# Optimization experiments

Hardware: AMD Instinct MI355X
Metric: run time of the kernel (lower is better)

The kernel has to match this reference:

```python
import jax, jax.numpy as jnp
import numpy as np

N = 100000      # nodes
E = 1600000     # edges (avg degree 16)
IN = 128        # in_channels
H = 128         # hidden_channels
OUT = 64        # out_channels
NHID = 3        # num_layers (hidden->hidden SAGE convs)


def _lin(k, fan_out, fan_in):
    s = 1.0 / np.sqrt(fan_in)
    return jax.random.uniform(k, (fan_out, fan_in), jnp.float32, -s, s)


def setup_inputs() -> dict:
    key = jax.random.key(0)
    ks = jax.random.split(key, 12)
    x = jax.random.normal(ks[0], (N, IN), dtype=jnp.float32)
    edge_index = jax.random.randint(ks[1], (2, E), 0, N, dtype=jnp.int32)
    # inProj Linear(IN -> H)
    Wp = _lin(ks[2], H, IN)
    bp = jnp.zeros((H,), jnp.float32)
    # 3 hidden SAGEConv(H -> H): lin_l (with bias) on aggregated neighbors, lin_r (no bias) on root
    Wl_h = jnp.stack([_lin(jax.random.fold_in(ks[3], i), H, H) for i in range(NHID)])
    bl_h = jnp.zeros((NHID, H), jnp.float32)
    Wr_h = jnp.stack([_lin(jax.random.fold_in(ks[4], i), H, H) for i in range(NHID)])
    # output SAGEConv(H -> OUT)
    Wl_o = _lin(ks[5], OUT, H)
    bl_o = jnp.zeros((OUT,), jnp.float32)
    Wr_o = _lin(ks[6], OUT, H)
    return {"x": x, "edge_index": edge_index, "Wp": Wp, "bp": bp,
            "Wl_h": Wl_h, "bl_h": bl_h, "Wr_h": Wr_h,
            "Wl_o": Wl_o, "bl_o": bl_o, "Wr_o": Wr_o}


def reference(x, edge_index, Wp, bp, Wl_h, bl_h, Wr_h, Wl_o, bl_o, Wr_o):
    src, dst = edge_index[0], edge_index[1]
    ones = jnp.ones((E,), x.dtype)
    deg = jax.ops.segment_sum(ones, dst, num_segments=N)           # [N]
    inv_deg = (1.0 / jnp.maximum(deg, 1.0))[:, None]               # [N,1]

    def sage(h, Wl, bl, Wr):
        # mean aggregation of source features onto destinations (irregular gather+scatter)
        s = jax.ops.segment_sum(h[src], dst, num_segments=N)       # [N,d]
        mean = s * inv_deg
        return mean @ Wl.T + bl + h @ Wr.T

    h = x @ Wp.T + bp
    inp = h
    h = jax.nn.relu(h)
    for i in range(NHID):
        h = sage(h, Wl_h[i], bl_h[i], Wr_h[i])
        h = jax.nn.relu(h)                                          # dropout is identity in eval
        h = h + 0.2 * inp
    h = sage(h, Wl_o, bl_o, Wr_o)
    return jax.nn.log_softmax(h, axis=-1)
```

## Files before the change

kernel.cpp:

```cpp
#include <hip/hip_runtime.h>
#include <math.h>

#define N_NODES 100000
#define N_EDGES 1600000
#define NBUK 391
#define PCHUNK 8192
#define NPBLK 196
#define PBLK16 3128

typedef unsigned short u16;
typedef unsigned char u8;
typedef __bf16 bf16x8 __attribute__((ext_vector_type(8)));
typedef float f32x4 __attribute__((ext_vector_type(4)));
typedef float f32x2 __attribute__((ext_vector_type(2)));

#define OFF_RP      0u
#define OFF_INVDEG  400016u
#define OFF_BHIST   800016u
#define OFF_BBASE   801600u
#define OFF_GCUR    803200u
#define OFF_PCTR    804800u
#define OFF_PAIRS   805056u
#define OFF_COL     13605056u
#define OFF_PACK    20005056u
#define OFF_INP     20267200u
#define OFF_H       45867200u
#define OFF_H8A     71467200u
#define OFF_H8B     84267200u
#define OFF_GL      97067200u
#define OFF_GR      109867200u
#define OFF_MEAN    122667200u
#define WS_NEEDED   148267200u

#define PK_WP   0
#define PK_WL   16384
#define PK_WR   65536
#define PK_WLO  114688
#define PK_WRO  122880

__device__ __forceinline__ float bfl(unsigned u) {
  union { unsigned i; float f; } v; v.i = u << 16; return v.f;
}
__device__ __forceinline__ float bfh(unsigned u) {
  union { unsigned i; float f; } v; v.i = u & 0xFFFF0000u; return v.f;
}
__device__ __forceinline__ u16 f2b(float f) {
  union { float f; unsigned i; } v; v.f = f;
  unsigned r = (v.i + 0x7FFFu + ((v.i >> 16) & 1u)) >> 16;
  return (u16)r;
}

__global__ __launch_bounds__(256) void pack_weights_k(
    const float* __restrict__ Wp, const float* __restrict__ Wl,
    const float* __restrict__ Wr, const float* __restrict__ Wlo,
    const float* __restrict__ Wro, u16* __restrict__ P) {
  int t = blockIdx.x * 256 + threadIdx.x;
  if (t >= 16384) return;
  const float* W; u16* dst; int j; int NT;
  if (t < 2048)        { W = Wp;                    dst = P + PK_WP;                j = t;                 NT = 8; }
  else if (t < 8192)   { int m = (t - 2048) >> 11;  j = (t - 2048) & 2047;
                         W = Wl + (m << 14);        dst = P + PK_WL + (m << 14);    NT = 8; }
  else if (t < 14336)  { int m = (t - 8192) >> 11;  j = (t - 8192) & 2047;
                         W = Wr + (m << 14);        dst = P + PK_WR + (m << 14);    NT = 8; }
  else if (t < 15360)  { j = t - 14336;             W = Wlo;  dst = P + PK_WLO;     NT = 4; }
  else                 { j = t - 15360;             W = Wro;  dst = P + PK_WRO;     NT = 4; }
  int lane = j & 63;
  int nt, kt;
  if (NT == 8) { nt = (j >> 6) & 7; kt = j >> 9; }
  else         { nt = (j >> 6) & 3; kt = j >> 8; }
  int n  = nt * 16 + (lane & 15);
  int k0 = kt * 32 + ((lane >> 4) << 3);
  const float* s = W + n * 128 + k0;
  ushort4 lo = make_ushort4(f2b(s[0]), f2b(s[1]), f2b(s[2]), f2b(s[3]));
  ushort4 hi = make_ushort4(f2b(s[4]), f2b(s[5]), f2b(s[6]), f2b(s[7]));
  *(ushort4*)(dst + j * 8)     = lo;
  *(ushort4*)(dst + j * 8 + 4) = hi;
}

__global__ __launch_bounds__(256) void bhist_k(const int* __restrict__ dst,
                                               int* __restrict__ bhist) {
  __shared__ int lc[NBUK];
  int t = threadIdx.x;
  for (int i = t; i < NBUK; i += 256) lc[i] = 0;
  __syncthreads();
  int base = blockIdx.x * 4096;
#pragma unroll
  for (int r = 0; r < 16; r++) {
    int i = base + r * 256 + t;
    if (i < N_EDGES) atomicAdd(&lc[dst[i] >> 8], 1);
  }
  __syncthreads();
  for (int i = t; i < NBUK; i += 256)
    if (lc[i]) atomicAdd(&bhist[i], lc[i]);
}

__global__ __launch_bounds__(512) void bscan_k(const int* __restrict__ bhist,
                                               int* __restrict__ bbase,
                                               int* __restrict__ gcur,
                                               int* __restrict__ rp) {
  __shared__ int s[512];
  int t = threadIdx.x;
  int v = (t < NBUK) ? bhist[t] : 0;
  s[t] = v;
  __syncthreads();
  for (int off = 1; off < 512; off <<= 1) {
    int u = (t >= off) ? s[t - off] : 0;
    __syncthreads();
    s[t] += u;
    __syncthreads();
  }
  if (t < NBUK) { int e = s[t] - v; bbase[t] = e; gcur[t] = e; }
  if (t == NBUK - 1) { bbase[NBUK] = s[t]; rp[N_NODES] = s[t]; }
}

__global__ __launch_bounds__(256) void part_k(const int* __restrict__ src,
                                              const int* __restrict__ dst,
                                              int* __restrict__ gcur,
                                              uint2* __restrict__ pairs) {
  __shared__ int lcnt[NBUK + 1];
  __shared__ int lofs[512];
  __shared__ int cur[NBUK];
  __shared__ int gslot[NBUK];
  __shared__ uint2 stag[PCHUNK];
  int t = threadIdx.x;
  for (int i = t; i < NBUK + 1; i += 256) lcnt[i] = 0;
  __syncthreads();
  int base = blockIdx.x * PCHUNK;
#pragma unroll
  for (int r = 0; r < PCHUNK / 256; r++) {
    int i = base + r * 256 + t;
    if (i < N_EDGES) atomicAdd(&lcnt[dst[i] >> 8], 1);
  }
  __syncthreads();
  {
    int e1 = t + 256;
    lofs[t]  = (t  <= NBUK) ? lcnt[t]  : 0;
    lofs[e1] = (e1 <= NBUK) ? lcnt[e1] : 0;
    __syncthreads();
    for (int off = 1; off < 512; off <<= 1) {
      int a0 = (t  >= off) ? lofs[t  - off] : 0;
      int a1 = (e1 >= off) ? lofs[e1 - off] : 0;
      __syncthreads();
      lofs[t] += a0; lofs[e1] += a1;
      __syncthreads();
    }
    int o0 = lofs[t]  - ((t  <= NBUK) ? lcnt[t]  : 0);
    int o1 = lofs[e1] - ((e1 <= NBUK) ? lcnt[e1] : 0);
    __syncthreads();
    lofs[t] = o0; lofs[e1] = o1;
    __syncthreads();
  }
  for (int i = t; i < NBUK; i += 256) cur[i] = lofs[i];
  __syncthreads();
#pragma unroll
  for (int r = 0; r < PCHUNK / 256; r++) {
    int i = base + r * 256 + t;
    if (i < N_EDGES) {
      int d = dst[i];
      int slot = atomicAdd(&cur[d >> 8], 1);
      stag[slot] = make_uint2((unsigned)src[i], (unsigned)d);
    }
  }
  __syncthreads();
  for (int i = t; i < NBUK; i += 256)
    if (lcnt[i]) gslot[i] = atomicAdd(&gcur[i], lcnt[i]);
  __syncthreads();
  int total = lofs[NBUK];
  for (int p = t; p < total; p += 256) {
    uint2 pr = stag[p];
    int b = (int)(pr.y >> 8);
    pairs[gslot[b] + (p - lofs[b])] = pr;
  }
}

__global__ __launch_bounds__(256) void csr_k(const uint2* __restrict__ pairs,
                                             const int* __restrict__ bbase,
                                             int* __restrict__ rp,
                                             float* __restrict__ invdeg,
                                             int* __restrict__ col) {
  __shared__ int cnt[256];
  __shared__ int scn[256];
  __shared__ int cur[256];
  int b = blockIdx.x, t = threadIdx.x;
  int lo = bbase[b], hi = bbase[b + 1];
  cnt[t] = 0;
  __syncthreads();
  for (int p = lo + t; p < hi; p += 256)
    atomicAdd(&cnt[pairs[p].y & 255], 1);
  __syncthreads();
  int c = cnt[t];
  scn[t] = c;
  __syncthreads();
  for (int off = 1; off < 256; off <<= 1) {
    int v = (t >= off) ? scn[t - off] : 0;
    __syncthreads();
    scn[t] += v;
    __syncthreads();
  }
  int excl = scn[t] - c;
  int node = (b << 8) + t;
  if (node < N_NODES) {
    rp[node] = lo + excl;
    invdeg[node] = 1.0f / (float)(c > 1 ? c : 1);
  }
  cur[t] = lo + excl;
  __syncthreads();
  for (int p = lo + t; p < hi; p += 256) {
    uint2 pr = pairs[p];
    int slot = atomicAdd(&cur[pr.y & 255], 1);
    col[slot] = (int)pr.x;
  }
}

__global__ __launch_bounds__(256) void aggregate_plane16_k(
    const u8* __restrict__ h8, const int* __restrict__ rp,
    const int* __restrict__ col, const float* __restrict__ invdeg,
    u16* __restrict__ mean) {
  int b = blockIdx.x;
  int plane = (b & 7) >> 1;
  int idx = ((b >> 3) << 1) + (b & 1);
  int tid = threadIdx.x;
  int grp = tid >> 1, lane2 = tid & 1;
  int node = idx * 128 + grp;
  if (node >= N_NODES) return;
  int beg = rp[node], end = rp[node + 1];
  const u8* hp = h8 + (size_t)plane * (N_NODES * 32) + lane2 * 16;
  f32x2 av[8];
#pragma unroll
  for (int i = 0; i < 8; i++) av[i] = (f32x2){0.f, 0.f};
  int j = beg;
  for (; j + 8 <= end; j += 8) {
    int4 ci = *(const int4*)(col + j + lane2 * 4);
    int cia[4] = {ci.x, ci.y, ci.z, ci.w};
    uint4 v[8];
#pragma unroll
    for (int e = 0; e < 8; e++) {
      int s = __shfl(cia[e & 3], e >> 2, 2);
      v[e] = *(const uint4*)(hp + ((size_t)(unsigned)s << 5));
    }
#pragma unroll
    for (int e = 0; e < 8; e++) {
      av[0] += __builtin_amdgcn_cvt_pk_f32_fp8(v[e].x, false);
      av[1] += __builtin_amdgcn_cvt_pk_f32_fp8(v[e].x, true);
      av[2] += __builtin_amdgcn_cvt_pk_f32_fp8(v[e].y, false);
      av[3] += __builtin_amdgcn_cvt_pk_f32_fp8(v[e].y, true);
      av[4] += __builtin_amdgcn_cvt_pk_f32_fp8(v[e].z, false);
      av[5] += __builtin_amdgcn_cvt_pk_f32_fp8(v[e].z, true);
      av[6] += __builtin_amdgcn_cvt_pk_f32_fp8(v[e].w, false);
      av[7] += __builtin_amdgcn_cvt_pk_f32_fp8(v[e].w, true);
    }
  }
  for (; j < end; j++) {
    int s = col[j];
    uint4 vv = *(const uint4*)(hp + ((size_t)(unsigned)s << 5));
    av[0] += __builtin_amdgcn_cvt_pk_f32_fp8(vv.x, false);
    av[1] += __builtin_amdgcn_cvt_pk_f32_fp8(vv.x, true);
    av[2] += __builtin_amdgcn_cvt_pk_f32_fp8(vv.y, false);
    av[3] += __builtin_amdgcn_cvt_pk_f32_fp8(vv.y, true);
    av[4] += __builtin_amdgcn_cvt_pk_f32_fp8(vv.z, false);
    av[5] += __builtin_amdgcn_cvt_pk_f32_fp8(vv.z, true);
    av[6] += __builtin_amdgcn_cvt_pk_f32_fp8(vv.w, false);
    av[7] += __builtin_amdgcn_cvt_pk_f32_fp8(vv.w, true);
  }
  float wd = invdeg[node];
  u16* mp = mean + (size_t)plane * (N_NODES * 32) + (size_t)node * 32 + lane2 * 16;
  *(ushort4*)(mp)      = make_ushort4(f2b(av[0][0]*wd), f2b(av[0][1]*wd), f2b(av[1][0]*wd), f2b(av[1][1]*wd));
  *(ushort4*)(mp + 4)  = make_ushort4(f2b(av[2][0]*wd), f2b(av[2][1]*wd), f2b(av[3][0]*wd), f2b(av[3][1]*wd));
  *(ushort4*)(mp + 8)  = make_ushort4(f2b(av[4][0]*wd), f2b(av[4][1]*wd), f2b(av[5][0]*wd), f2b(av[5][1]*wd));
  *(ushort4*)(mp + 12) = make_ushort4(f2b(av[6][0]*wd), f2b(av[6][1]*wd), f2b(av[7][0]*wd), f2b(av[7][1]*wd));
}

__global__ __launch_bounds__(256) void out_gather16_k(
    const u16* __restrict__ gl, const int* __restrict__ rp,
    const int* __restrict__ col, const float* __restrict__ invdeg,
    float* __restrict__ partial) {
  int b = blockIdx.x;
  int plane = (b & 7) >> 1;
  int idx = ((b >> 3) << 1) + (b & 1);
  int tid = threadIdx.x;
  int grp = tid >> 1, lane2 = tid & 1;
  int node = idx * 128 + grp;
  if (node >= N_NODES) return;
  int beg = rp[node], end = rp[node + 1];
  const u16* gp = gl + (size_t)plane * (N_NODES * 16) + lane2 * 8;
  float a[8];
#pragma unroll
  for (int i = 0; i < 8; i++) a[i] = 0.f;
  int j = beg;
  for (; j + 8 <= end; j += 8) {
    int4 ci = *(const int4*)(col + j + lane2 * 4);
    int cia[4] = {ci.x, ci.y, ci.z, ci.w};
    uint4 v[8];
#pragma unroll
    for (int e = 0; e < 8; e++) {
      int s = __shfl(cia[e & 3], e >> 2, 2);
      v[e] = *(const uint4*)(gp + ((size_t)(unsigned)s << 4));
    }
#pragma unroll
    for (int e = 0; e < 8; e++) {
      a[0] += bfl(v[e].x); a[1] += bfh(v[e].x);
      a[2] += bfl(v[e].y); a[3] += bfh(v[e].y);
      a[4] += bfl(v[e].z); a[5] += bfh(v[e].z);
      a[6] += bfl(v[e].w); a[7] += bfh(v[e].w);
    }
  }
  for (; j < end; j++) {
    int s = col[j];
    uint4 vv = *(const uint4*)(gp + ((size_t)(unsigned)s << 4));
    a[0] += bfl(vv.x); a[1] += bfh(vv.x);
    a[2] += bfl(vv.y); a[3] += bfh(vv.y);
    a[4] += bfl(vv.z); a[5] += bfh(vv.z);
    a[6] += bfl(vv.w); a[7] += bfh(vv.w);
  }
  float wd = invdeg[node];
  float* pp = partial + (size_t)node * 64 + plane * 16 + lane2 * 8;
  *(float4*)(pp)     = make_float4(a[0]*wd, a[1]*wd, a[2]*wd, a[3]*wd);
  *(float4*)(pp + 4) = make_float4(a[4]*wd, a[5]*wd, a[6]*wd, a[7]*wd);
}

__global__ __launch_bounds__(256) void out_softmax_k(
    const float* __restrict__ partial, const u16* __restrict__ gr,
    const float* __restrict__ blo, float* __restrict__ outp) {
  int node = blockIdx.x * 8 + (threadIdx.x >> 5);
  int lane = threadIdx.x & 31;
  if (node >= N_NODES) return;
  float2 pz = *(const float2*)(partial + (size_t)node * 64 + lane * 2);
  unsigned g = *(const unsigned*)(gr + (size_t)node * 64 + lane * 2);
  float z0 = pz.x + bfl(g) + blo[lane * 2];
  float z1 = pz.y + bfh(g) + blo[lane * 2 + 1];
  float mx = fmaxf(z0, z1);
#pragma unroll
  for (int off = 16; off >= 1; off >>= 1) mx = fmaxf(mx, __shfl_xor(mx, off, 32));
  float s = __expf(z0 - mx) + __expf(z1 - mx);
#pragma unroll
  for (int off = 16; off >= 1; off >>= 1) s += __shfl_xor(s, off, 32);
  float ro = mx + __logf(s);
  float2 o = make_float2(z0 - ro, z1 - ro);
  *(float2*)(outp + (size_t)node * 64 + lane * 2) = o;
}

__global__ __launch_bounds__(256) void inproj_mfma_k(
    const float* __restrict__ X, const u16* __restrict__ P,
    const float* __restrict__ bias,
    u16* __restrict__ inp, u16* __restrict__ hout, u8* __restrict__ h8out, int M) {
  __shared__ float zb[64 * 132];
  int tid = threadIdx.x;
  int w = tid >> 6, lane = tid & 63;
  int quad = lane >> 4, l15 = lane & 15;
  int m0 = blockIdx.x * 64;
  int rowa = m0 + w * 16 + l15; if (rowa > M - 1) rowa = M - 1;
  f32x4 acc[8] = {};
#pragma unroll
  for (int kt = 0; kt < 4; kt++) {
    const float* xr = X + (long)rowa * 128 + kt * 32 + quad * 8;
    float4 p0 = *(const float4*)xr;
    float4 p1 = *(const float4*)(xr + 4);
    union { ushort4 u4[2]; bf16x8 v; } fa;
    fa.u4[0] = make_ushort4(f2b(p0.x), f2b(p0.y), f2b(p0.z), f2b(p0.w));
    fa.u4[1] = make_ushort4(f2b(p1.x), f2b(p1.y), f2b(p1.z), f2b(p1.w));
    const u16* pb = P + ((kt * 8) * 64 + lane) * 8;
#pragma unroll
    for (int nt = 0; nt < 8; nt++) {
      bf16x8 bf = *(const bf16x8*)(pb + nt * 512);
      acc[nt] = __builtin_amdgcn_mfma_f32_16x16x32_bf16(fa.v, bf, acc[nt], 0, 0, 0);
    }
  }
#pragma unroll
  for (int nt = 0; nt < 8; nt++) {
    int c = nt * 16 + l15;
    float b = bias[c];
#pragma unroll
    for (int r = 0; r < 4; r++)
      zb[(w * 16 + quad * 4 + r) * 132 + c] = acc[nt][r] + b;
  }
  __syncthreads();
  int r = lane >> 2, seg = lane & 3;
  long grow = m0 + w * 16 + r;
  if (grow < M) {
    const float* zrow = &zb[(w * 16 + r) * 132 + seg * 32];
    u16* ip = inp + grow * 128 + seg * 32;
    u16* hp = hout + grow * 128 + seg * 32;
    u8*  qp = h8out + (size_t)seg * (N_NODES * 32) + grow * 32;
#pragma unroll
    for (int b = 0; b < 4; b++) {
      float zv[8];
      *(float4*)&zv[0] = *(const float4*)(zrow + b * 8);
      *(float4*)&zv[4] = *(const float4*)(zrow + b * 8 + 4);
      float rv[8];
#pragma unroll
      for (int jj = 0; jj < 8; jj++) rv[jj] = fmaxf(zv[jj], 0.f);
      *(ushort4*)(ip + b * 8)     = make_ushort4(f2b(zv[0]), f2b(zv[1]), f2b(zv[2]), f2b(zv[3]));
      *(ushort4*)(ip + b * 8 + 4) = make_ushort4(f2b(zv[4]), f2b(zv[5]), f2b(zv[6]), f2b(zv[7]));
      *(ushort4*)(hp + b * 8)     = make_ushort4(f2b(rv[0]), f2b(rv[1]), f2b(rv[2]), f2b(rv[3]));
      *(ushort4*)(hp + b * 8 + 4) = make_ushort4(f2b(rv[4]), f2b(rv[5]), f2b(rv[6]), f2b(rv[7]));
      unsigned q0 = 0, q1 = 0;
      q0 = __builtin_amdgcn_cvt_pk_fp8_f32(rv[0], rv[1], q0, false);
      q0 = __builtin_amdgcn_cvt_pk_fp8_f32(rv[2], rv[3], q0, true);
      q1 = __builtin_amdgcn_cvt_pk_fp8_f32(rv[4], rv[5], q1, false);
      q1 = __builtin_amdgcn_cvt_pk_fp8_f32(rv[6], rv[7], q1, true);
      *(uint2*)(qp + b * 8) = make_uint2(q0, q1);
    }
  }
}

__global__ __launch_bounds__(256) void sage_mfma8_k(
    const u16* __restrict__ A0, const u16* __restrict__ P0,
    const u16* __restrict__ A1, const u16* __restrict__ P1,
    const float* __restrict__ bias, const u16* __restrict__ inp,
    u16* __restrict__ outp, u8* __restrict__ h8out, int M) {
  __shared__ float zb[64 * 132];
  int tid = threadIdx.x;
  int w = tid >> 6, lane = tid & 63;
  int quad = lane >> 4, l15 = lane & 15;
  int m0 = blockIdx.x * 64;
  int rowa = m0 + w * 16 + l15; if (rowa > M - 1) rowa = M - 1;
  f32x4 acc[8] = {};
#pragma unroll
  for (int kt = 0; kt < 4; kt++) {
    bf16x8 am = *(const bf16x8*)(A0 + (size_t)kt * (N_NODES * 32) + (size_t)rowa * 32 + quad * 8);
    bf16x8 ar = *(const bf16x8*)(A1 + (long)rowa * 128 + kt * 32 + quad * 8);
    const u16* pl = P0 + ((kt * 8) * 64 + lane) * 8;
    const u16* pr = P1 + ((kt * 8) * 64 + lane) * 8;
#pragma unroll
    for (int nt = 0; nt < 8; nt++) {
      bf16x8 b0 = *(const bf16x8*)(pl + nt * 512);
      bf16x8 b1 = *(const bf16x8*)(pr + nt * 512);
      acc[nt] = __builtin_amdgcn_mfma_f32_16x16x32_bf16(am, b0, acc[nt], 0, 0, 0);
      acc[nt] = __builtin_amdgcn_mfma_f32_16x16x32_bf16(ar, b1, acc[nt], 0, 0, 0);
    }
  }
#pragma unroll
  for (int nt = 0; nt < 8; nt++) {
    int c = nt * 16 + l15;
    float b = bias[c];
#pragma unroll
    for (int r = 0; r < 4; r++)
      zb[(w * 16 + quad * 4 + r) * 132 + c] = fmaxf(acc[nt][r] + b, 0.f);
  }
  __syncthreads();
  int r = lane >> 2, seg = lane & 3;
  long grow = m0 + w * 16 + r;
  if (grow < M) {
    const float* zrow = &zb[(w * 16 + r) * 132 + seg * 32];
    const u16* ip = inp + grow * 128 + seg * 32;
    u16* op = outp + grow * 128 + seg * 32;
#pragma unroll
    for (int b = 0; b < 4; b++) {
      float zv[8];
      *(float4*)&zv[0] = *(const float4*)(zrow + b * 8);
      *(float4*)&zv[4] = *(const float4*)(zrow + b * 8 + 4);
      uint2 iv0 = *(const uint2*)(ip + b * 8);
      uint2 iv1 = *(const uint2*)(ip + b * 8 + 4);
      float fv[8];
      fv[0] = zv[0] + 0.2f * bfl(iv0.x); fv[1] = zv[1] + 0.2f * bfh(iv0.x);
      fv[2] = zv[2] + 0.2f * bfl(iv0.y); fv[3] = zv[3] + 0.2f * bfh(iv0.y);
      fv[4] = zv[4] + 0.2f * bfl(iv1.x); fv[5] = zv[5] + 0.2f * bfh(iv1.x);
      fv[6] = zv[6] + 0.2f * bfl(iv1.y); fv[7] = zv[7] + 0.2f * bfh(iv1.y);
      *(ushort4*)(op + b * 8)     = make_ushort4(f2b(fv[0]), f2b(fv[1]), f2b(fv[2]), f2b(fv[3]));
      *(ushort4*)(op + b * 8 + 4) = make_ushort4(f2b(fv[4]), f2b(fv[5]), f2b(fv[6]), f2b(fv[7]));
      if (h8out) {
        unsigned q0 = 0, q1 = 0;
        q0 = __builtin_amdgcn_cvt_pk_fp8_f32(fv[0], fv[1], q0, false);
        q0 = __builtin_amdgcn_cvt_pk_fp8_f32(fv[2], fv[3], q0, true);
        q1 = __builtin_amdgcn_cvt_pk_fp8_f32(fv[4], fv[5], q1, false);
        q1 = __builtin_amdgcn_cvt_pk_fp8_f32(fv[6], fv[7], q1, true);
        *(uint2*)(h8out + (size_t)seg * (N_NODES * 32) + grow * 32 + b * 8) = make_uint2(q0, q1);
      }
    }
  }
}

__global__ __launch_bounds__(256) void out_proj_k(
    const u16* __restrict__ A, const u16* __restrict__ PLO,
    const u16* __restrict__ PRO, u16* __restrict__ gl, u16* __restrict__ gr, int M) {
  __shared__ float zb[64 * 132];
  int tid = threadIdx.x;
  int w = tid >> 6, lane = tid & 63;
  int quad = lane >> 4, l15 = lane & 15;
  int m0 = blockIdx.x * 64;
  int rowa = m0 + w * 16 + l15; if (rowa > M - 1) rowa = M - 1;
  f32x4 acc[8] = {};
#pragma unroll
  for (int kt = 0; kt < 4; kt++) {
    bf16x8 af = *(const bf16x8*)(A + (long)rowa * 128 + kt * 32 + quad * 8);
#pragma unroll
    for (int nt = 0; nt < 4; nt++) {
      bf16x8 b0 = *(const bf16x8*)(PLO + ((kt * 4 + nt) * 64 + lane) * 8);
      bf16x8 b1 = *(const bf16x8*)(PRO + ((kt * 4 + nt) * 64 + lane) * 8);
      acc[nt]     = __builtin_amdgcn_mfma_f32_16x16x32_bf16(af, b0, acc[nt], 0, 0, 0);
      acc[4 + nt] = __builtin_amdgcn_mfma_f32_16x16x32_bf16(af, b1, acc[4 + nt], 0, 0, 0);
    }
  }
#pragma unroll
  for (int nt = 0; nt < 4; nt++) {
    int c = nt * 16 + l15;
#pragma unroll
    for (int r = 0; r < 4; r++) {
      zb[(w * 16 + quad * 4 + r) * 132 + c]      = acc[nt][r];
      zb[(w * 16 + quad * 4 + r) * 132 + 64 + c] = acc[4 + nt][r];
    }
  }
  __syncthreads();
  int r = lane >> 2, seg = lane & 3;
  long grow = m0 + w * 16 + r;
  if (grow < M) {
    const float* zrow = &zb[(w * 16 + r) * 132 + seg * 32];
#pragma unroll
    for (int b = 0; b < 4; b++) {
      float zv[8];
      *(float4*)&zv[0] = *(const float4*)(zrow + b * 8);
      *(float4*)&zv[4] = *(const float4*)(zrow + b * 8 + 4);
      u16* dp;
      if (seg < 2) {
        int plane = seg * 2 + (b >> 1);
        dp = gl + (size_t)plane * (N_NODES * 16) + grow * 16 + (b & 1) * 8;
      } else {
        dp = gr + grow * 64 + (seg - 2) * 32 + b * 8;
      }
      *(ushort4*)(dp)     = make_ushort4(f2b(zv[0]), f2b(zv[1]), f2b(zv[2]), f2b(zv[3]));
      *(ushort4*)(dp + 4) = make_ushort4(f2b(zv[4]), f2b(zv[5]), f2b(zv[6]), f2b(zv[7]));
    }
  }
}

extern "C" void kernel_launch(void* const* d_in, const int* in_sizes, int n_in,
                              void* d_out, int out_size, void* d_ws, size_t ws_size,
                              hipStream_t stream) {
  if (ws_size < (size_t)WS_NEEDED) return;
  const float* x   = (const float*)d_in[0];
  const int*   ei  = (const int*)d_in[1];
  const float* Wp  = (const float*)d_in[2];
  const float* bp  = (const float*)d_in[3];
  const float* Wl  = (const float*)d_in[4];
  const float* bl  = (const float*)d_in[5];
  const float* Wr  = (const float*)d_in[6];
  const float* Wlo = (const float*)d_in[7];
  const float* blo = (const float*)d_in[8];
  const float* Wro = (const float*)d_in[9];
  float* out = (float*)d_out;
  char* ws = (char*)d_ws;
  int*   rp     = (int*)(ws + OFF_RP);
  float* invdeg = (float*)(ws + OFF_INVDEG);
  int*   bhist  = (int*)(ws + OFF_BHIST);
  int*   bbase  = (int*)(ws + OFF_BBASE);
  int*   gcur   = (int*)(ws + OFF_GCUR);
  uint2* pairs  = (uint2*)(ws + OFF_PAIRS);
  int*   col    = (int*)(ws + OFF_COL);
  u16*   pack   = (u16*)(ws + OFF_PACK);
  u16*   inp    = (u16*)(ws + OFF_INP);
  u16*   h      = (u16*)(ws + OFF_H);
  u8*    h8a    = (u8*)(ws + OFF_H8A);
  u8*    h8b    = (u8*)(ws + OFF_H8B);
  u16*   gl     = (u16*)(ws + OFF_GL);
  u16*   gr     = (u16*)(ws + OFF_GR);
  u16*   mean   = (u16*)(ws + OFF_MEAN);
  float* partial = (float*)(ws + OFF_MEAN);
  const int* srcv = ei;
  const int* dstv = ei + N_EDGES;

  hipMemsetAsync(ws + OFF_BHIST, 0, OFF_PAIRS - OFF_BHIST, stream);
  pack_weights_k<<<64, 256, 0, stream>>>(Wp, Wl, Wr, Wlo, Wro, pack);
  bhist_k<<<391, 256, 0, stream>>>(dstv, bhist);
  bscan_k<<<1, 512, 0, stream>>>(bhist, bbase, gcur, rp);
  part_k<<<NPBLK, 256, 0, stream>>>(srcv, dstv, gcur, pairs);
  csr_k<<<NBUK, 256, 0, stream>>>(pairs, bbase, rp, invdeg, col);

  int gblk = (N_NODES + 63) / 64;
  int fblk = (N_NODES + 7) / 8;

  inproj_mfma_k<<<gblk, 256, 0, stream>>>(x, pack + PK_WP, bp, inp, h, h8a, N_NODES);

  aggregate_plane16_k<<<PBLK16, 256, 0, stream>>>(h8a, rp, col, invdeg, mean);
  sage_mfma8_k<<<gblk, 256, 0, stream>>>(mean, pack + PK_WL, h, pack + PK_WR,
                                         bl, inp, h, h8b, N_NODES);
  aggregate_plane16_k<<<PBLK16, 256, 0, stream>>>(h8b, rp, col, invdeg, mean);
  sage_mfma8_k<<<gblk, 256, 0, stream>>>(mean, pack + PK_WL + 16384, h, pack + PK_WR + 16384,
                                         bl + 128, inp, h, h8a, N_NODES);
  aggregate_plane16_k<<<PBLK16, 256, 0, stream>>>(h8a, rp, col, invdeg, mean);
  sage_mfma8_k<<<gblk, 256, 0, stream>>>(mean, pack + PK_WL + 32768, h, pack + PK_WR + 32768,
                                         bl + 256, inp, h, (u8*)nullptr, N_NODES);

  out_proj_k<<<gblk, 256, 0, stream>>>(h, pack + PK_WLO, pack + PK_WRO, gl, gr, N_NODES);
  out_gather16_k<<<PBLK16, 256, 0, stream>>>(gl, rp, col, invdeg, partial);
  out_softmax_k<<<fblk, 256, 0, stream>>>(partial, gr, blo, out);
}
```

Before: 540.2 us.

## Build CSR with per-node degree atomics and direct scatter instead of bucket partition

Replaces the two-level bucketed partition (bucket histogram, block-local staging of src/dst pairs, per-bucket CSR build) with a per-node degree count via global atomics, a two-level prefix scan, and a direct atomic scatter of source ids into col. This removes the intermediate pairs array and its extra read/write passes. The trade-off is heavier global atomic traffic on random addresses. Within-row neighbor order is also no longer deterministic, which can change the locality of the later gathers.

```diff
diff --git a/kernel.cpp b/kernel.cpp
--- a/kernel.cpp
+++ b/kernel.cpp
@@ -4,9 +4,8 @@
 #define N_NODES 100000
 #define N_EDGES 1600000
 #define NBUK 391
-#define PCHUNK 8192
-#define NPBLK 196
 #define PBLK16 3128
+#define EBLK 1563
 
 typedef unsigned short u16;
 typedef unsigned char u8;
@@ -20,7 +19,8 @@
 #define OFF_BBASE   801600u
 #define OFF_GCUR    803200u
 #define OFF_PCTR    804800u
-#define OFF_PAIRS   805056u
+#define OFF_DEG     805056u
+#define OFF_CUR     1205056u
 #define OFF_COL     13605056u
 #define OFF_PACK    20005056u
 #define OFF_INP     20267200u
@@ -77,26 +77,41 @@
   *(ushort4*)(dst + j * 8 + 4) = hi;
 }
 
-__global__ __launch_bounds__(256) void bhist_k(const int* __restrict__ dst,
+__global__ __launch_bounds__(256) void deg_k(const int* __restrict__ dst,
+                                             int* __restrict__ deg) {
+  int i = (blockIdx.x * 256 + threadIdx.x) * 4;
+  if (i + 3 >= N_EDGES) {
+    for (; i < N_EDGES; i++) atomicAdd(&deg[dst[i]], 1);
+    return;
+  }
+  int4 d = *(const int4*)(dst + i);
+  atomicAdd(&deg[d.x], 1);
+  atomicAdd(&deg[d.y], 1);
+  atomicAdd(&deg[d.z], 1);
+  atomicAdd(&deg[d.w], 1);
+}
+
+__global__ __launch_bounds__(256) void scan1_k(const int* __restrict__ deg,
+                                               int* __restrict__ rp,
                                                int* __restrict__ bhist) {
-  __shared__ int lc[NBUK];
-  int t = threadIdx.x;
-  for (int i = t; i < NBUK; i += 256) lc[i] = 0;
+  __shared__ int s[256];
+  int b = blockIdx.x, t = threadIdx.x;
+  int node = b * 256 + t;
+  int v = (node < N_NODES) ? deg[node] : 0;
+  s[t] = v;
   __syncthreads();
-  int base = blockIdx.x * 4096;
-#pragma unroll
-  for (int r = 0; r < 16; r++) {
-    int i = base + r * 256 + t;
-    if (i < N_EDGES) atomicAdd(&lc[dst[i] >> 8], 1);
-  }
-  __syncthreads();
-  for (int i = t; i < NBUK; i += 256)
-    if (lc[i]) atomicAdd(&bhist[i], lc[i]);
+  for (int off = 1; off < 256; off <<= 1) {
+    int u = (t >= off) ? s[t - off] : 0;
+    __syncthreads();
+    s[t] += u;
+    __syncthreads();
+  }
+  if (t == 255) bhist[b] = s[255];
+  if (node < N_NODES) rp[node] = s[t] - v;
 }
 
 __global__ __launch_bounds__(512) void bscan_k(const int* __restrict__ bhist,
                                                int* __restrict__ bbase,
-                                               int* __restrict__ gcur,
                                                int* __restrict__ rp) {
   __shared__ int s[512];
   int t = threadIdx.x;
@@ -109,107 +124,47 @@
     s[t] += u;
     __syncthreads();
   }
-  if (t < NBUK) { int e = s[t] - v; bbase[t] = e; gcur[t] = e; }
-  if (t == NBUK - 1) { bbase[NBUK] = s[t]; rp[N_NODES] = s[t]; }
-}
-
-__global__ __launch_bounds__(256) void part_k(const int* __restrict__ src,
-                                              const int* __restrict__ dst,
-                                              int* __restrict__ gcur,
-                                              uint2* __restrict__ pairs) {
-  __shared__ int lcnt[NBUK + 1];
-  __shared__ int lofs[512];
-  __shared__ int cur[NBUK];
-  __shared__ int gslot[NBUK];
-  __shared__ uint2 stag[PCHUNK];
-  int t = threadIdx.x;
-  for (int i = t; i < NBUK + 1; i += 256) lcnt[i] = 0;
-  __syncthreads();
-  int base = blockIdx.x * PCHUNK;
-#pragma unroll
-  for (int r = 0; r < PCHUNK / 256; r++) {
-    int i = base + r * 256 + t;
-    if (i < N_EDGES) atomicAdd(&lcnt[dst[i] >> 8], 1);
-  }
-  __syncthreads();
-  {
-    int e1 = t + 256;
-    lofs[t]  = (t  <= NBUK) ? lcnt[t]  : 0;
-    lofs[e1] = (e1 <= NBUK) ? lcnt[e1] : 0;
-    __syncthreads();
-    for (int off = 1; off < 512; off <<= 1) {
-      int a0 = (t  >= off) ? lofs[t  - off] : 0;
-      int a1 = (e1 >= off) ? lofs[e1 - off] : 0;
-      __syncthreads();
-      lofs[t] += a0; lofs[e1] += a1;
-      __syncthreads();
-    }
-    int o0 = lofs[t]  - ((t  <= NBUK) ? lcnt[t]  : 0);
-    int o1 = lofs[e1] - ((e1 <= NBUK) ? lcnt[e1] : 0);
-    __syncthreads();
-    lofs[t] = o0; lofs[e1] = o1;
-    __syncthreads();
-  }
-  for (int i = t; i < NBUK; i += 256) cur[i] = lofs[i];
-  __syncthreads();
-#pragma unroll
-  for (int r = 0; r < PCHUNK / 256; r++) {
-    int i = base + r * 256 + t;
-    if (i < N_EDGES) {
-      int d = dst[i];
-      int slot = atomicAdd(&cur[d >> 8], 1);
-      stag[slot] = make_uint2((unsigned)src[i], (unsigned)d);
-    }
-  }
-  __syncthreads();
-  for (int i = t; i < NBUK; i += 256)
-    if (lcnt[i]) gslot[i] = atomicAdd(&gcur[i], lcnt[i]);
-  __syncthreads();
-  int total = lofs[NBUK];
-  for (int p = t; p < total; p += 256) {
-    uint2 pr = stag[p];
-    int b = (int)(pr.y >> 8);
-    pairs[gslot[b] + (p - lofs[b])] = pr;
-  }
-}
-
-__global__ __launch_bounds__(256) void csr_k(const uint2* __restrict__ pairs,
-                                             const int* __restrict__ bbase,
-                                             int* __restrict__ rp,
-                                             float* __restrict__ invdeg,
-                                             int* __restrict__ col) {
-  __shared__ int cnt[256];
-  __shared__ int scn[256];
-  __shared__ int cur[256];
+  if (t < NBUK) bbase[t] = s[t] - v;
+  if (t == NBUK - 1) rp[N_NODES] = s[t];
+}
+
+__global__ __launch_bounds__(256) void scan2_k(const int* __restrict__ bbase,
+                                               const int* __restrict__ deg,
+                                               int* __restrict__ rp,
+                                               int* __restrict__ cur,
+                                               float* __restrict__ invdeg) {
   int b = blockIdx.x, t = threadIdx.x;
-  int lo = bbase[b], hi = bbase[b + 1];
-  cnt[t] = 0;
-  __syncthreads();
-  for (int p = lo + t; p < hi; p += 256)
-    atomicAdd(&cnt[pairs[p].y & 255], 1);
-  __syncthreads();
-  int c = cnt[t];
-  scn[t] = c;
-  __syncthreads();
-  for (int off = 1; off < 256; off <<= 1) {
-    int v = (t >= off) ? scn[t - off] : 0;
-    __syncthreads();
-    scn[t] += v;
-    __syncthreads();
-  }
-  int excl = scn[t] - c;
-  int node = (b << 8) + t;
-  if (node < N_NODES) {
-    rp[node] = lo + excl;
-    invdeg[node] = 1.0f / (float)(c > 1 ? c : 1);
-  }
-  cur[t] = lo + excl;
-  __syncthreads();
-  for (int p = lo + t; p < hi; p += 256) {
-    uint2 pr = pairs[p];
-    int slot = atomicAdd(&cur[pr.y & 255], 1);
-    col[slot] = (int)pr.x;
-  }
+  int node = b * 256 + t;
+  if (node >= N_NODES) return;
+  int r = rp[node] + bbase[b];
+  rp[node] = r;
+  cur[node] = r;
+  int d = deg[node];
+  invdeg[node] = 1.0f / (float)(d > 1 ? d : 1);
+}
+
+__global__ __launch_bounds__(256) void scatter_k(const int* __restrict__ src,
+                                                 const int* __restrict__ dst,
+                                                 int* __restrict__ cur,
+                                                 int* __restrict__ col) {
+  int i = (blockIdx.x * 256 + threadIdx.x) * 4;
+  if (i + 3 >= N_EDGES) {
+    for (; i < N_EDGES; i++) {
+      int p = atomicAdd(&cur[dst[i]], 1);
+      col[p] = src[i];
+    }
+    return;
+  }
+  int4 s4 = *(const int4*)(src + i);
+  int4 d4 = *(const int4*)(dst + i);
+  int p0 = atomicAdd(&cur[d4.x], 1);
+  int p1 = atomicAdd(&cur[d4.y], 1);
+  int p2 = atomicAdd(&cur[d4.z], 1);
+  int p3 = atomicAdd(&cur[d4.w], 1);
+  col[p0] = s4.x;
+  col[p1] = s4.y;
+  col[p2] = s4.z;
+  col[p3] = s4.w;
 }
 
 __global__ __launch_bounds__(256) void aggregate_plane16_k(
@@ -543,8 +498,8 @@
   float* invdeg = (float*)(ws + OFF_INVDEG);
   int*   bhist  = (int*)(ws + OFF_BHIST);
   int*   bbase  = (int*)(ws + OFF_BBASE);
-  int*   gcur   = (int*)(ws + OFF_GCUR);
-  uint2* pairs  = (uint2*)(ws + OFF_PAIRS);
+  int*   deg    = (int*)(ws + OFF_DEG);
+  int*   cur    = (int*)(ws + OFF_CUR);
   int*   col    = (int*)(ws + OFF_COL);
   u16*   pack   = (u16*)(ws + OFF_PACK);
   u16*   inp    = (u16*)(ws + OFF_INP);
@@ -558,12 +513,14 @@
   const int* srcv = ei;
   const int* dstv = ei + N_EDGES;
 
-  hipMemsetAsync(ws + OFF_BHIST, 0, OFF_PAIRS - OFF_BHIST, stream);
+  hipMemsetAsync(ws + OFF_BHIST, 0, OFF_DEG - OFF_BHIST, stream);
+  hipMemsetAsync(ws + OFF_DEG, 0, 400016u, stream);
   pack_weights_k<<<64, 256, 0, stream>>>(Wp, Wl, Wr, Wlo, Wro, pack);
-  bhist_k<<<391, 256, 0, stream>>>(dstv, bhist);
-  bscan_k<<<1, 512, 0, stream>>>(bhist, bbase, gcur, rp);
-  part_k<<<NPBLK, 256, 0, stream>>>(srcv, dstv, gcur, pairs);
-  csr_k<<<NBUK, 256, 0, stream>>>(pairs, bbase, rp, invdeg, col);
+  deg_k<<<EBLK, 256, 0, stream>>>(dstv, deg);
+  scan1_k<<<NBUK, 256, 0, stream>>>(deg, rp, bhist);
+  bscan_k<<<1, 512, 0, stream>>>(bhist, bbase, rp);
+  scan2_k<<<NBUK, 256, 0, stream>>>(bbase, deg, rp, cur, invdeg);
+  scatter_k<<<EBLK, 256, 0, stream>>>(srcv, dstv, cur, col);
 
   int gblk = (N_NODES + 63) / 64;
   int fblk = (N_NODES + 7) / 8;
```

Result: slower. 663.0 us (+22.7%).
